# Kernel tuning notes

Measured on AMD Instinct MI355X. Metric: run time of the kernel, lower is better.

## Reference

```python
import jax, jax.numpy as jnp
import numpy as np

N = 100000      # entity nodes
E = 1000000     # edges per relation
D_IN = 256
HID = 128
EPS = 1e-16     # PyG softmax denominator eps
NEG_SLOPE = 0.2 # GATConv default leaky_relu slope


def _gat_conv(x, ei, Ws, Wd, a_s, a_d, b):
    """Single-head GATConv (heads=1, concat=False) with self-loops."""
    n = x.shape[0]
    loop = jnp.arange(n, dtype=ei.dtype)
    src = jnp.concatenate([ei[0], loop])  # [E+N]
    dst = jnp.concatenate([ei[1], loop])
    h_src = x @ Ws                         # [N, HID]
    h_dst = x @ Wd                         # [N, HID]
    a_src = h_src @ a_s                    # [N]
    a_dst = h_dst @ a_d                    # [N]
    e = jax.nn.leaky_relu(a_src[src] + a_dst[dst], NEG_SLOPE)  # [E+N]
    # numerically-stable softmax over incoming edges of each dst node
    m = jax.ops.segment_max(e, dst, num_segments=n)
    ex = jnp.exp(e - m[dst])
    denom = jax.ops.segment_sum(ex, dst, num_segments=n)
    alpha = ex / (denom[dst] + EPS)        # [E+N]
    out = jax.ops.segment_sum(alpha[:, None] * h_src[src], dst, num_segments=n)
    return out + b


def setup_inputs() -> dict:
    key = jax.random.key(0)
    ks = jax.random.split(key, 9)
    s_in = 1.0 / np.sqrt(D_IN)
    s_h = 1.0 / np.sqrt(HID)
    return {
        "x": jax.random.normal(ks[0], (N, D_IN), dtype=jnp.float32),
        "edge_index_r0": jax.random.randint(ks[1], (2, E), 0, N, dtype=jnp.int64)
                         if jax.config.jax_enable_x64 else jax.random.randint(ks[1], (2, E), 0, N).astype(jnp.int32),
        "edge_index_r1": jax.random.randint(ks[2], (2, E), 0, N, dtype=jnp.int64)
                         if jax.config.jax_enable_x64 else jax.random.randint(ks[2], (2, E), 0, N).astype(jnp.int32),
        "W_src": jax.random.normal(ks[3], (2, D_IN, HID), dtype=jnp.float32) * s_in,
        "W_dst": jax.random.normal(ks[4], (2, D_IN, HID), dtype=jnp.float32) * s_in,
        "att_src": jax.random.normal(ks[5], (2, HID), dtype=jnp.float32) * s_h,
        "att_dst": jax.random.normal(ks[6], (2, HID), dtype=jnp.float32) * s_h,
        "bias": jnp.zeros((2, HID), dtype=jnp.float32),
    }


def reference(x, edge_index_r0, edge_index_r1, W_src, W_dst, att_src, att_dst, bias):
    # HeteroConv aggr='sum' over the two entity->entity relations
    out = _gat_conv(x, edge_index_r0, W_src[0], W_dst[0], att_src[0], att_dst[0], bias[0])
    out = out + _gat_conv(x, edge_index_r1, W_src[1], W_dst[1], att_src[1], att_dst[1], bias[1])
    # ELU; dropout p=0.0 is identity
    return jax.nn.elu(out)
```

## Files before the change

kernel.cpp:

```cpp
#include <hip/hip_runtime.h>

typedef __attribute__((ext_vector_type(8))) __bf16 bf16x8;
typedef __attribute__((ext_vector_type(4))) float floatx4;
typedef __attribute__((ext_vector_type(2))) float floatx2;

__device__ __forceinline__ float bf2f(unsigned short u) {
    return __uint_as_float(((unsigned)u) << 16);
}
__device__ __forceinline__ unsigned short f2bf(float f) {
    unsigned u = __float_as_uint(f);
    unsigned r = u + 0x7FFFu + ((u >> 16) & 1u);
    return (unsigned short)(r >> 16);
}

__global__ void detect_k(const unsigned short* __restrict__ xs, int* __restrict__ flag) {
    __shared__ int sred[256];
    int tid = threadIdx.x;
    int cnt = 0;
    for (int j = 0; j < 16; ++j) {
        unsigned short u = xs[(tid * 16 + j) * 2];
        int e = (u >> 7) & 0xFF;
        cnt += (e >= 96 && e <= 159) ? 1 : 0;
    }
    sred[tid] = cnt;
    __syncthreads();
    for (int s = 128; s > 0; s >>= 1) {
        if (tid < s) sred[tid] += sred[tid + s];
        __syncthreads();
    }
    if (tid == 0) *flag = (sred[0] > 2048) ? 1 : 0;
}

__device__ __forceinline__ void canon8(const void* src, unsigned short* dst,
                                       long long idx, int f) {
    if (f) {
        *(uint4*)&dst[idx] = *(const uint4*)((const unsigned short*)src + idx);
    } else {
        const float* sf = (const float*)src;
        unsigned short v[8];
        for (int j = 0; j < 8; ++j) v[j] = f2bf(sf[idx + j]);
        *(uint4*)&dst[idx] = *(const uint4*)v;
    }
}

__global__ void prep_k(const void* __restrict__ Ws, const void* __restrict__ Wd,
                       const void* __restrict__ as, const void* __restrict__ ad,
                       const void* __restrict__ b,
                       unsigned short* __restrict__ Bt,
                       unsigned short* __restrict__ bsb,
                       float* __restrict__ vecs, const int* __restrict__ flag) {
    int blk = blockIdx.x, tid = threadIdx.x;
    int f = *flag;
    if (blk < 256) {
        int i = blk * 256 + tid;
        int r = i >> 15, rem = i & 32767;
        int k = rem >> 7, nn = rem & 127;
        unsigned short w = f ? ((const unsigned short*)Ws)[i]
                             : f2bf(((const float*)Ws)[i]);
        Bt[(size_t)r * 32768 + nn * 256 + k] = w;
    } else if (blk < 258) {
        int r = blk - 256;
        int k = tid;
        float s = 0.f, t = 0.f;
        if (f) {
            const unsigned short* wsrow = (const unsigned short*)Ws + (size_t)r * 32768 + (size_t)k * 128;
            const unsigned short* wdrow = (const unsigned short*)Wd + (size_t)r * 32768 + (size_t)k * 128;
            const unsigned short* asr = (const unsigned short*)as + r * 128;
            const unsigned short* adr = (const unsigned short*)ad + r * 128;
            for (int h = 0; h < 128; ++h) {
                s += bf2f(wsrow[h]) * bf2f(asr[h]);
                t += bf2f(wdrow[h]) * bf2f(adr[h]);
            }
        } else {
            const float* wsrow = (const float*)Ws + (size_t)r * 32768 + (size_t)k * 128;
            const float* wdrow = (const float*)Wd + (size_t)r * 32768 + (size_t)k * 128;
            const float* asr = (const float*)as + r * 128;
            const float* adr = (const float*)ad + r * 128;
            for (int h = 0; h < 128; ++h) {
                s += wsrow[h] * asr[h];
                t += wdrow[h] * adr[h];
            }
        }
        vecs[(r * 2 + 0) * 256 + k] = s;
        vecs[(r * 2 + 1) * 256 + k] = t;
    } else {
        if (tid < 32) canon8(b, bsb, (long long)tid * 8, f);
    }
}

__global__ __launch_bounds__(256) void a_canon_k(const void* __restrict__ xraw,
                                                 unsigned short* __restrict__ xb,
                                                 const float* __restrict__ vecs,
                                                 float* __restrict__ aout, int n,
                                                 const int* __restrict__ flag) {
    __shared__ float sv[1024];
    int tid = threadIdx.x;
    for (int j = 0; j < 4; ++j) sv[j * 256 + tid] = vecs[j * 256 + tid];
    __syncthreads();
    int lane = tid & 63, wave = tid >> 6;
    int row = blockIdx.x * 4 + wave;
    if (row >= n) return;
    float xf[4];
    if (*flag) {
        uint2 u = *(const uint2*)((const unsigned short*)xraw + (size_t)row * 256 + lane * 4);
        xf[0] = bf2f((unsigned short)(u.x & 0xFFFF));
        xf[1] = bf2f((unsigned short)(u.x >> 16));
        xf[2] = bf2f((unsigned short)(u.y & 0xFFFF));
        xf[3] = bf2f((unsigned short)(u.y >> 16));
        *(uint2*)&xb[(size_t)row * 256 + lane * 4] = u;
    } else {
        float4 f = *(const float4*)((const float*)xraw + (size_t)row * 256 + lane * 4);
        xf[0] = f.x; xf[1] = f.y; xf[2] = f.z; xf[3] = f.w;
        unsigned short v[4] = {f2bf(f.x), f2bf(f.y), f2bf(f.z), f2bf(f.w)};
        *(uint2*)&xb[(size_t)row * 256 + lane * 4] = *(const uint2*)v;
    }
    float s[4] = {0.f, 0.f, 0.f, 0.f};
    for (int j = 0; j < 4; ++j)
        for (int q = 0; q < 4; ++q)
            s[j] += xf[q] * sv[j * 256 + lane * 4 + q];
    for (int j = 0; j < 4; ++j)
        for (int off = 32; off > 0; off >>= 1)
            s[j] += __shfl_down(s[j], off);
    if (lane == 0)
        for (int j = 0; j < 4; ++j) aout[(size_t)j * n + row] = s[j];
}

__device__ __forceinline__ void gload_lds16(const void* g, void* l) {
    __builtin_amdgcn_global_load_lds((const __attribute__((address_space(1))) void*)g,
                                     (__attribute__((address_space(3))) void*)l, 16, 0, 0);
}

__global__ __launch_bounds__(256) void gemm_h(const unsigned short* __restrict__ x,
                                              const unsigned short* __restrict__ Btg,
                                              unsigned short* __restrict__ hout, int n) {
    const int r = blockIdx.y;
    const unsigned short* bt = Btg + (size_t)r * 32768;
    unsigned short* h = hout + (size_t)r * n * 128;
    const int r0 = blockIdx.x * 128;
    __shared__ __align__(16) unsigned short As[128 * 64];
    __shared__ __align__(16) unsigned short Bs[128 * 64];
    int tid = threadIdx.x;
    int lane = tid & 63, wave = tid >> 6;
    int wm = wave >> 1, wn = wave & 1;

    floatx4 acc[4][4];
    for (int mt = 0; mt < 4; ++mt)
        for (int nt = 0; nt < 4; ++nt)
            acc[mt][nt] = (floatx4){0.f, 0.f, 0.f, 0.f};

    int srow = lane >> 3;
    int q    = lane & 7;
    int m16  = lane & 15;
    int qb   = lane >> 4;

    for (int k0 = 0; k0 < 256; k0 += 64) {
        for (int i = 0; i < 4; ++i) {
            int L = wave * 4 + i;
            int row = L * 8 + srow;
            int sw = ((q ^ (row & 7)) << 3);
            gload_lds16(x + (size_t)(r0 + row) * 256 + k0 + sw, &As[L * 512]);
            gload_lds16(bt + (size_t)row * 256 + k0 + sw, &Bs[L * 512]);
        }
        __syncthreads();
        for (int s = 0; s < 2; ++s) {
            int qr = qb + s * 4;
            bf16x8 af[4], bfv[4];
            for (int mt = 0; mt < 4; ++mt) {
                int row = wm * 64 + mt * 16 + m16;
                af[mt] = *(const bf16x8*)&As[row * 64 + ((qr ^ (row & 7)) << 3)];
            }
            for (int nt = 0; nt < 4; ++nt) {
                int row = wn * 64 + nt * 16 + m16;
                bfv[nt] = *(const bf16x8*)&Bs[row * 64 + ((qr ^ (row & 7)) << 3)];
            }
            for (int mt = 0; mt < 4; ++mt)
                for (int nt = 0; nt < 4; ++nt)
                    acc[mt][nt] = __builtin_amdgcn_mfma_f32_16x16x32_bf16(
                        af[mt], bfv[nt], acc[mt][nt], 0, 0, 0);
        }
        __syncthreads();
    }
    for (int mt = 0; mt < 4; ++mt) {
        int baser = r0 + wm * 64 + mt * 16 + qb * 4;
        for (int nt = 0; nt < 4; ++nt) {
            int c = wn * 64 + nt * 16 + m16;
            for (int i = 0; i < 4; ++i) {
                int gr = baser + i;
                if (gr < n) h[(size_t)gr * 128 + c] = f2bf(acc[mt][nt][i]);
            }
        }
    }
}

__global__ void hist2_k(const int* __restrict__ ei0, const int* __restrict__ ei1,
                        int* __restrict__ cnt0, int* __restrict__ cnt1,
                        int* __restrict__ rank0, int* __restrict__ rank1,
                        int E_, int n) {
    int rel = blockIdx.y;
    const int* ei = rel ? ei1 : ei0;
    int* cnt = rel ? cnt1 : cnt0;
    int* rank = rel ? rank1 : rank0;
    int t = blockIdx.x * 256 + threadIdx.x;
    if (t >= E_ + n) return;
    int d = (t < E_) ? ei[E_ + t] : (t - E_);
    rank[t] = atomicAdd(&cnt[d], 1);
}

__global__ __launch_bounds__(256) void scan_red_k(const int* __restrict__ cnt0,
                                                  const int* __restrict__ cnt1,
                                                  int* __restrict__ part,
                                                  int n, int nb) {
    __shared__ int s[256];
    int rel = blockIdx.y;
    const int* cnt = rel ? cnt1 : cnt0;
    int i = blockIdx.x * 256 + threadIdx.x;
    s[threadIdx.x] = (i < n) ? cnt[i] : 0;
    __syncthreads();
    for (int o = 128; o > 0; o >>= 1) {
        if (threadIdx.x < o) s[threadIdx.x] += s[threadIdx.x + o];
        __syncthreads();
    }
    if (threadIdx.x == 0) part[rel * nb + blockIdx.x] = s[0];
}

__global__ __launch_bounds__(1024) void scan_mid_k(int* __restrict__ part, int nb) {
    __shared__ int s[1024];
    int rel = blockIdx.x;
    int t = threadIdx.x;
    s[t] = (t < nb) ? part[rel * nb + t] : 0;
    __syncthreads();
    for (int o = 1; o < 1024; o <<= 1) {
        int v = (t >= o) ? s[t - o] : 0;
        __syncthreads();
        s[t] += v;
        __syncthreads();
    }
    if (t < nb) part[rel * nb + t] = (t == 0) ? 0 : s[t - 1];
}

__global__ __launch_bounds__(256) void scan_off_k(const int* __restrict__ cnt0,
                                                  const int* __restrict__ cnt1,
                                                  const int* __restrict__ part,
                                                  int* __restrict__ off0,
                                                  int* __restrict__ off1,
                                                  int n, int nb) {
    __shared__ int s[256];
    int rel = blockIdx.y;
    const int* cnt = rel ? cnt1 : cnt0;
    int* off = rel ? off1 : off0;
    int i = blockIdx.x * 256 + threadIdx.x;
    int t = threadIdx.x;
    int v = (i < n) ? cnt[i] : 0;
    s[t] = v;
    __syncthreads();
    for (int o = 1; o < 256; o <<= 1) {
        int u = (t >= o) ? s[t - o] : 0;
        __syncthreads();
        s[t] += u;
        __syncthreads();
    }
    if (i < n) off[i] = part[rel * nb + blockIdx.x] + s[t] - v;
}

__global__ void fill2_k(const int* __restrict__ ei0, const int* __restrict__ ei1,
                        const float* __restrict__ avals,
                        const int* __restrict__ off0, const int* __restrict__ off1,
                        const int* __restrict__ rank0, const int* __restrict__ rank1,
                        unsigned long long* __restrict__ pair0,
                        unsigned long long* __restrict__ pair1,
                        int E_, int n) {
    int rel = blockIdx.y;
    const int* ei = rel ? ei1 : ei0;
    const float* as_ = avals + (rel ? 2 * (size_t)n : 0);
    const float* ad_ = avals + (rel ? 3 * (size_t)n : (size_t)n);
    const int* off = rel ? off1 : off0;
    const int* rank = rel ? rank1 : rank0;
    unsigned long long* pair = rel ? pair1 : pair0;
    int t = blockIdx.x * 256 + threadIdx.x;
    if (t >= E_ + n) return;
    int s, d;
    if (t < E_) { s = ei[t]; d = ei[E_ + t]; } else { s = t - E_; d = s; }
    float e = as_[s] + ad_[d];
    e = e > 0.f ? e : 0.2f * e;
    float w = __expf(e);
    int pos = off[d] + rank[t];
    pair[pos] = ((unsigned long long)__float_as_uint(w) << 32) | (unsigned)s;
}

__device__ __forceinline__ void acc8pk(floatx2* a, float w, const uint4& hv) {
    floatx2 wv = {w, w};
    const unsigned u[4] = {hv.x, hv.y, hv.z, hv.w};
#pragma unroll
    for (int k = 0; k < 4; ++k) {
        floatx2 hf;
        hf.x = __uint_as_float(u[k] << 16);
        hf.y = __uint_as_float(u[k] & 0xFFFF0000u);
        asm("v_pk_fma_f32 %0, %1, %2, %0" : "+v"(a[k]) : "v"(wv), "v"(hf));
    }
}

__global__ __launch_bounds__(256) void agg_k(
    const int* __restrict__ off0, const int* __restrict__ cnt0,
    const unsigned long long* __restrict__ pair0,
    const int* __restrict__ off1, const int* __restrict__ cnt1,
    const unsigned long long* __restrict__ pair1,
    const char* __restrict__ h0, const char* __restrict__ h1,
    const unsigned short* __restrict__ bias, void* __restrict__ out,
    int n, const int* __restrict__ flag) {
    int wave = threadIdx.x >> 6, lane = threadIdx.x & 63;
    int g = lane >> 4, l = lane & 15;
    unsigned l4 = (unsigned)l << 4;
    int d = blockIdx.x * 4 + wave;
    if (d >= n) return;

    int sA = off0[d], degA = cnt0[d];
    int sB = off1[d], degB = cnt1[d];
    int lastA = sA + degA - 1, lastB = sB + degB - 1;
    int nItA = (degA + 7) >> 3, nItB = (degB + 7) >> 3;
    int nIt = max(nItA, nItB);

    float denA = 0.f, denB = 0.f;
    floatx2 aA[4], aB[4];
#pragma unroll
    for (int k = 0; k < 4; ++k) {
        aA[k] = (floatx2){0.f, 0.f};
        aB[k] = (floatx2){0.f, 0.f};
    }

    int iA = sA + g, iB = sB + g;
    unsigned long long pA0 = pair0[min(iA, lastA)];
    unsigned long long pA1 = pair0[min(iA + 4, lastA)];
    unsigned long long pB0 = pair1[min(iB, lastB)];
    unsigned long long pB1 = pair1[min(iB + 4, lastB)];

    for (int it = 0; it < nIt; ++it) {
        uint4 hA0 = *(const uint4*)(h0 + ((((unsigned)pA0) << 8) + l4));
        uint4 hA1 = *(const uint4*)(h0 + ((((unsigned)pA1) << 8) + l4));
        uint4 hB0 = *(const uint4*)(h1 + ((((unsigned)pB0) << 8) + l4));
        uint4 hB1 = *(const uint4*)(h1 + ((((unsigned)pB1) << 8) + l4));
        float wA0 = (iA     <= lastA) ? __uint_as_float((unsigned)(pA0 >> 32)) : 0.f;
        float wA1 = (iA + 4 <= lastA) ? __uint_as_float((unsigned)(pA1 >> 32)) : 0.f;
        float wB0 = (iB     <= lastB) ? __uint_as_float((unsigned)(pB0 >> 32)) : 0.f;
        float wB1 = (iB + 4 <= lastB) ? __uint_as_float((unsigned)(pB1 >> 32)) : 0.f;
        iA += 8; iB += 8;
        pA0 = pair0[min(iA, lastA)];
        pA1 = pair0[min(iA + 4, lastA)];
        pB0 = pair1[min(iB, lastB)];
        pB1 = pair1[min(iB + 4, lastB)];
        denA += wA0 + wA1;
        denB += wB0 + wB1;
        acc8pk(aA, wA0, hA0);
        acc8pk(aA, wA1, hA1);
        acc8pk(aB, wB0, hB0);
        acc8pk(aB, wB1, hB1);
    }

    denA += __shfl_xor(denA, 16);
    denA += __shfl_xor(denA, 32);
    denB += __shfl_xor(denB, 16);
    denB += __shfl_xor(denB, 32);
    float invA = __builtin_amdgcn_rcpf(denA + 1e-16f);
    float invB = __builtin_amdgcn_rcpf(denB + 1e-16f);
    floatx2 ivA = {invA, invA}, ivB = {invB, invB};
#pragma unroll
    for (int k = 0; k < 4; ++k) {
        asm("v_pk_mul_f32 %0, %0, %1" : "+v"(aA[k]) : "v"(ivA));
        asm("v_pk_fma_f32 %0, %1, %2, %0" : "+v"(aA[k]) : "v"(aB[k]), "v"(ivB));
    }
    float t8[8] = {aA[0].x, aA[0].y, aA[1].x, aA[1].y,
                   aA[2].x, aA[2].y, aA[3].x, aA[3].y};

    uint4 b0 = *(const uint4*)&bias[l * 8];
    uint4 b1 = *(const uint4*)&bias[128 + l * 8];
    const unsigned* b0u = (const unsigned*)&b0;
    const unsigned* b1u = (const unsigned*)&b1;
    float v[8];
#pragma unroll
    for (int j = 0; j < 8; ++j) {
        float s = t8[j];
        s += __shfl_xor(s, 16);
        s += __shfl_xor(s, 32);
        unsigned w0 = b0u[j >> 1], w1 = b1u[j >> 1];
        float bb = bf2f((unsigned short)((j & 1) ? (w0 >> 16) : (w0 & 0xFFFFu)))
                 + bf2f((unsigned short)((j & 1) ? (w1 >> 16) : (w1 & 0xFFFFu)));
        float t = s + bb;
        v[j] = t > 0.f ? t : (__expf(t) - 1.f);
    }
    if (g == 0) {
        if (*flag) {
            unsigned pk[4];
            for (int j = 0; j < 4; ++j)
                pk[j] = ((unsigned)f2bf(v[2 * j + 1]) << 16) | (unsigned)f2bf(v[2 * j]);
            ((uint4*)out)[(size_t)d * 16 + l] = *(const uint4*)pk;
        } else {
            float4 f0 = make_float4(v[0], v[1], v[2], v[3]);
            float4 f1 = make_float4(v[4], v[5], v[6], v[7]);
            ((float4*)out)[(size_t)d * 32 + l * 2] = f0;
            ((float4*)out)[(size_t)d * 32 + l * 2 + 1] = f1;
        }
    }
}

static inline char* carve(char*& p, size_t bytes) {
    char* r = p;
    p += (bytes + 255) & ~(size_t)255;
    return r;
}

extern "C" void kernel_launch(void* const* d_in, const int* in_sizes, int n_in,
                              void* d_out, int out_size, void* d_ws, size_t ws_size,
                              hipStream_t stream) {
    (void)n_in; (void)out_size; (void)ws_size;
    const void* x_raw  = d_in[0];
    const int*  ei0    = (const int*)d_in[1];
    const int*  ei1    = (const int*)d_in[2];
    const void* Ws_raw = d_in[3];
    const void* Wd_raw = d_in[4];
    const void* as_raw = d_in[5];
    const void* ad_raw = d_in[6];
    const void* b_raw  = d_in[7];

    const int n = in_sizes[0] / 256;
    const int e = in_sizes[1] / 2;
    const int tot = e + n;
    const int nb = (n + 255) / 256;

    char* p = (char*)d_ws;
    float* avals = (float*)carve(p, (size_t)4 * n * 4);
    int*   cnt0  = (int*)carve(p, (size_t)2 * n * 4);
    int*   cnt1  = cnt0 + n;
    int*   off0  = (int*)carve(p, (size_t)n * 4);
    int*   off1  = (int*)carve(p, (size_t)n * 4);
    int*   part  = (int*)carve(p, (size_t)2 * nb * 4);
    int*   rank0 = (int*)carve(p, (size_t)tot * 4);
    int*   rank1 = (int*)carve(p, (size_t)tot * 4);
    unsigned long long* pair0 = (unsigned long long*)carve(p, (size_t)tot * 8);
    unsigned long long* pair1 = (unsigned long long*)carve(p, (size_t)tot * 8);
    float* vecs  = (float*)carve(p, 1024 * 4);
    int*   flag  = (int*)carve(p, 256);
    unsigned short* xb  = (unsigned short*)carve(p, (size_t)(n + 128) * 256 * 2);
    unsigned short* h0  = (unsigned short*)carve(p, (size_t)2 * n * 128 * 2);
    unsigned short* h1  = h0 + (size_t)n * 128;
    unsigned short* Bt  = (unsigned short*)carve(p, 65536 * 2);
    unsigned short* bsb = (unsigned short*)carve(p, 256 * 2);

    hipMemsetAsync(cnt0, 0, (size_t)2 * n * 4, stream);

    detect_k<<<1, 256, 0, stream>>>((const unsigned short*)x_raw, flag);
    prep_k<<<259, 256, 0, stream>>>(Ws_raw, Wd_raw, as_raw, ad_raw, b_raw,
                                    Bt, bsb, vecs, flag);

    int gb = (tot + 255) / 256;
    hist2_k<<<dim3(gb, 2), 256, 0, stream>>>(ei0, ei1, cnt0, cnt1, rank0, rank1, e, n);
    scan_red_k<<<dim3(nb, 2), 256, 0, stream>>>(cnt0, cnt1, part, n, nb);
    scan_mid_k<<<2, 1024, 0, stream>>>(part, nb);
    scan_off_k<<<dim3(nb, 2), 256, 0, stream>>>(cnt0, cnt1, part, off0, off1, n, nb);

    a_canon_k<<<(n + 3) / 4, 256, 0, stream>>>(x_raw, xb, vecs, avals, n, flag);
    gemm_h<<<dim3((n + 127) / 128, 2), 256, 0, stream>>>(xb, Bt, h0, n);

    fill2_k<<<dim3(gb, 2), 256, 0, stream>>>(ei0, ei1, avals, off0, off1,
                                             rank0, rank1, pair0, pair1, e, n);

    agg_k<<<(n + 3) / 4, 256, 0, stream>>>(off0, cnt0, pair0, off1, cnt1, pair1,
                                           (const char*)h0, (const char*)h1,
                                           bsb, d_out, n, flag);
}
```

Measured before the change: 468.5 us.

## Merge independent launches into heterogeneous block-dispatch kernels to cut launch gaps

Merges detection with the attention-vector prep into one single-block kernel. Combines the histogram, x canonicalisation/attention dot products and W transpose into one grid partitioned by block index. Also fuses the GEMM with the edge fill pass, so independent work runs side by side and fewer kernel launch gaps and tail bubbles occur. In exchange, the mixed kernels carry the larger shared-memory footprint (the fill blocks now allocate the GEMM LDS), which may lower occupancy for the lightweight branches.

```diff
diff --git a/kernel.cpp b/kernel.cpp
--- a/kernel.cpp
+++ b/kernel.cpp
@@ -11,24 +11,6 @@
     unsigned u = __float_as_uint(f);
     unsigned r = u + 0x7FFFu + ((u >> 16) & 1u);
     return (unsigned short)(r >> 16);
-}
-
-__global__ void detect_k(const unsigned short* __restrict__ xs, int* __restrict__ flag) {
-    __shared__ int sred[256];
-    int tid = threadIdx.x;
-    int cnt = 0;
-    for (int j = 0; j < 16; ++j) {
-        unsigned short u = xs[(tid * 16 + j) * 2];
-        int e = (u >> 7) & 0xFF;
-        cnt += (e >= 96 && e <= 159) ? 1 : 0;
-    }
-    sred[tid] = cnt;
-    __syncthreads();
-    for (int s = 128; s > 0; s >>= 1) {
-        if (tid < s) sred[tid] += sred[tid + s];
-        __syncthreads();
-    }
-    if (tid == 0) *flag = (sred[0] > 2048) ? 1 : 0;
 }
 
 __device__ __forceinline__ void canon8(const void* src, unsigned short* dst,
@@ -43,24 +25,33 @@
     }
 }
 
-__global__ void prep_k(const void* __restrict__ Ws, const void* __restrict__ Wd,
-                       const void* __restrict__ as, const void* __restrict__ ad,
-                       const void* __restrict__ b,
-                       unsigned short* __restrict__ Bt,
-                       unsigned short* __restrict__ bsb,
-                       float* __restrict__ vecs, const int* __restrict__ flag) {
-    int blk = blockIdx.x, tid = threadIdx.x;
-    int f = *flag;
-    if (blk < 256) {
-        int i = blk * 256 + tid;
-        int r = i >> 15, rem = i & 32767;
-        int k = rem >> 7, nn = rem & 127;
-        unsigned short w = f ? ((const unsigned short*)Ws)[i]
-                             : f2bf(((const float*)Ws)[i]);
-        Bt[(size_t)r * 32768 + nn * 256 + k] = w;
-    } else if (blk < 258) {
-        int r = blk - 256;
-        int k = tid;
+__global__ __launch_bounds__(256) void detect2_k(
+    const unsigned short* __restrict__ xs,
+    const void* __restrict__ Ws, const void* __restrict__ Wd,
+    const void* __restrict__ as, const void* __restrict__ ad,
+    const void* __restrict__ b,
+    int* __restrict__ flag, float* __restrict__ vecs,
+    unsigned short* __restrict__ bsb) {
+    __shared__ int sred[256];
+    __shared__ int sflag;
+    int tid = threadIdx.x;
+    int cnt = 0;
+    for (int j = 0; j < 16; ++j) {
+        unsigned short u = xs[(tid * 16 + j) * 2];
+        int e = (u >> 7) & 0xFF;
+        cnt += (e >= 96 && e <= 159) ? 1 : 0;
+    }
+    sred[tid] = cnt;
+    __syncthreads();
+    for (int s = 128; s > 0; s >>= 1) {
+        if (tid < s) sred[tid] += sred[tid + s];
+        __syncthreads();
+    }
+    if (tid == 0) { sflag = (sred[0] > 2048) ? 1 : 0; *flag = sflag; }
+    __syncthreads();
+    int f = sflag;
+    int k = tid;
+    for (int r = 0; r < 2; ++r) {
         float s = 0.f, t = 0.f;
         if (f) {
             const unsigned short* wsrow = (const unsigned short*)Ws + (size_t)r * 32768 + (size_t)k * 128;
@@ -83,127 +74,74 @@
         }
         vecs[(r * 2 + 0) * 256 + k] = s;
         vecs[(r * 2 + 1) * 256 + k] = t;
-    } else {
-        if (tid < 32) canon8(b, bsb, (long long)tid * 8, f);
-    }
-}
-
-__global__ __launch_bounds__(256) void a_canon_k(const void* __restrict__ xraw,
-                                                 unsigned short* __restrict__ xb,
-                                                 const float* __restrict__ vecs,
-                                                 float* __restrict__ aout, int n,
-                                                 const int* __restrict__ flag) {
+    }
+    if (tid < 32) canon8(b, bsb, (long long)tid * 8, f);
+}
+
+__global__ __launch_bounds__(256) void mix1_k(
+    const int* __restrict__ ei0, const int* __restrict__ ei1,
+    int* __restrict__ cnt0, int* __restrict__ cnt1,
+    int* __restrict__ rank0, int* __restrict__ rank1, int E_, int histB,
+    const void* __restrict__ xraw, unsigned short* __restrict__ xb,
+    const float* __restrict__ vecs, float* __restrict__ aout, int n, int canB,
+    const void* __restrict__ Ws, unsigned short* __restrict__ Bt,
+    const int* __restrict__ flag) {
     __shared__ float sv[1024];
-    int tid = threadIdx.x;
-    for (int j = 0; j < 4; ++j) sv[j * 256 + tid] = vecs[j * 256 + tid];
-    __syncthreads();
-    int lane = tid & 63, wave = tid >> 6;
-    int row = blockIdx.x * 4 + wave;
-    if (row >= n) return;
-    float xf[4];
-    if (*flag) {
-        uint2 u = *(const uint2*)((const unsigned short*)xraw + (size_t)row * 256 + lane * 4);
-        xf[0] = bf2f((unsigned short)(u.x & 0xFFFF));
-        xf[1] = bf2f((unsigned short)(u.x >> 16));
-        xf[2] = bf2f((unsigned short)(u.y & 0xFFFF));
-        xf[3] = bf2f((unsigned short)(u.y >> 16));
-        *(uint2*)&xb[(size_t)row * 256 + lane * 4] = u;
-    } else {
-        float4 f = *(const float4*)((const float*)xraw + (size_t)row * 256 + lane * 4);
-        xf[0] = f.x; xf[1] = f.y; xf[2] = f.z; xf[3] = f.w;
-        unsigned short v[4] = {f2bf(f.x), f2bf(f.y), f2bf(f.z), f2bf(f.w)};
-        *(uint2*)&xb[(size_t)row * 256 + lane * 4] = *(const uint2*)v;
-    }
-    float s[4] = {0.f, 0.f, 0.f, 0.f};
-    for (int j = 0; j < 4; ++j)
-        for (int q = 0; q < 4; ++q)
-            s[j] += xf[q] * sv[j * 256 + lane * 4 + q];
-    for (int j = 0; j < 4; ++j)
-        for (int off = 32; off > 0; off >>= 1)
-            s[j] += __shfl_down(s[j], off);
-    if (lane == 0)
-        for (int j = 0; j < 4; ++j) aout[(size_t)j * n + row] = s[j];
-}
-
-__device__ __forceinline__ void gload_lds16(const void* g, void* l) {
-    __builtin_amdgcn_global_load_lds((const __attribute__((address_space(1))) void*)g,
-                                     (__attribute__((address_space(3))) void*)l, 16, 0, 0);
-}
-
-__global__ __launch_bounds__(256) void gemm_h(const unsigned short* __restrict__ x,
-                                              const unsigned short* __restrict__ Btg,
-                                              unsigned short* __restrict__ hout, int n) {
-    const int r = blockIdx.y;
-    const unsigned short* bt = Btg + (size_t)r * 32768;
-    unsigned short* h = hout + (size_t)r * n * 128;
-    const int r0 = blockIdx.x * 128;
-    __shared__ __align__(16) unsigned short As[128 * 64];
-    __shared__ __align__(16) unsigned short Bs[128 * 64];
-    int tid = threadIdx.x;
-    int lane = tid & 63, wave = tid >> 6;
-    int wm = wave >> 1, wn = wave & 1;
-
-    floatx4 acc[4][4];
-    for (int mt = 0; mt < 4; ++mt)
-        for (int nt = 0; nt < 4; ++nt)
-            acc[mt][nt] = (floatx4){0.f, 0.f, 0.f, 0.f};
-
-    int srow = lane >> 3;
-    int q    = lane & 7;
-    int m16  = lane & 15;
-    int qb   = lane >> 4;
-
-    for (int k0 = 0; k0 < 256; k0 += 64) {
-        for (int i = 0; i < 4; ++i) {
-            int L = wave * 4 + i;
-            int row = L * 8 + srow;
-            int sw = ((q ^ (row & 7)) << 3);
-            gload_lds16(x + (size_t)(r0 + row) * 256 + k0 + sw, &As[L * 512]);
-            gload_lds16(bt + (size_t)row * 256 + k0 + sw, &Bs[L * 512]);
+    int b = blockIdx.x, tid = threadIdx.x;
+    if (b < histB) {
+        int rel = b & 1;
+        int t = ((b >> 1) << 8) + tid;
+        if (t >= E_ + n) return;
+        const int* ei = rel ? ei1 : ei0;
+        int* cnt = rel ? cnt1 : cnt0;
+        int* rank = rel ? rank1 : rank0;
+        int d = (t < E_) ? ei[E_ + t] : (t - E_);
+        rank[t] = atomicAdd(&cnt[d], 1);
+        return;
+    }
+    b -= histB;
+    if (b < canB) {
+        for (int j = 0; j < 4; ++j) sv[j * 256 + tid] = vecs[j * 256 + tid];
+        __syncthreads();
+        int lane = tid & 63, wave = tid >> 6;
+        int row = b * 4 + wave;
+        if (row >= n) return;
+        float xf[4];
+        if (*flag) {
+            uint2 u = *(const uint2*)((const unsigned short*)xraw + (size_t)row * 256 + lane * 4);
+            xf[0] = bf2f((unsigned short)(u.x & 0xFFFF));
+            xf[1] = bf2f((unsigned short)(u.x >> 16));
+            xf[2] = bf2f((unsigned short)(u.y & 0xFFFF));
+            xf[3] = bf2f((unsigned short)(u.y >> 16));
+            *(uint2*)&xb[(size_t)row * 256 + lane * 4] = u;
+        } else {
+            float4 f = *(const float4*)((const float*)xraw + (size_t)row * 256 + lane * 4);
+            xf[0] = f.x; xf[1] = f.y; xf[2] = f.z; xf[3] = f.w;
+            unsigned short v[4] = {f2bf(f.x), f2bf(f.y), f2bf(f.z), f2bf(f.w)};
+            *(uint2*)&xb[(size_t)row * 256 + lane * 4] = *(const uint2*)v;
         }
-        __syncthreads();
-        for (int s = 0; s < 2; ++s) {
-            int qr = qb + s * 4;
-            bf16x8 af[4], bfv[4];
-            for (int mt = 0; mt < 4; ++mt) {
-                int row = wm * 64 + mt * 16 + m16;
-                af[mt] = *(const bf16x8*)&As[row * 64 + ((qr ^ (row & 7)) << 3)];
-            }
-            for (int nt = 0; nt < 4; ++nt) {
-                int row = wn * 64 + nt * 16 + m16;
-                bfv[nt] = *(const bf16x8*)&Bs[row * 64 + ((qr ^ (row & 7)) << 3)];
-            }
-            for (int mt = 0; mt < 4; ++mt)
-                for (int nt = 0; nt < 4; ++nt)
-                    acc[mt][nt] = __builtin_amdgcn_mfma_f32_16x16x32_bf16(
-                        af[mt], bfv[nt], acc[mt][nt], 0, 0, 0);
-        }
-        __syncthreads();
-    }
-    for (int mt = 0; mt < 4; ++mt) {
-        int baser = r0 + wm * 64 + mt * 16 + qb * 4;
-        for (int nt = 0; nt < 4; ++nt) {
-            int c = wn * 64 + nt * 16 + m16;
-            for (int i = 0; i < 4; ++i) {
-                int gr = baser + i;
-                if (gr < n) h[(size_t)gr * 128 + c] = f2bf(acc[mt][nt][i]);
-            }
-        }
-    }
-}
-
-__global__ void hist2_k(const int* __restrict__ ei0, const int* __restrict__ ei1,
-                        int* __restrict__ cnt0, int* __restrict__ cnt1,
-                        int* __restrict__ rank0, int* __restrict__ rank1,
-                        int E_, int n) {
-    int rel = blockIdx.y;
-    const int* ei = rel ? ei1 : ei0;
-    int* cnt = rel ? cnt1 : cnt0;
-    int* rank = rel ? rank1 : rank0;
-    int t = blockIdx.x * 256 + threadIdx.x;
-    if (t >= E_ + n) return;
-    int d = (t < E_) ? ei[E_ + t] : (t - E_);
-    rank[t] = atomicAdd(&cnt[d], 1);
+        float s[4] = {0.f, 0.f, 0.f, 0.f};
+        for (int j = 0; j < 4; ++j)
+            for (int q = 0; q < 4; ++q)
+                s[j] += xf[q] * sv[j * 256 + lane * 4 + q];
+        for (int j = 0; j < 4; ++j)
+            for (int off = 32; off > 0; off >>= 1)
+                s[j] += __shfl_down(s[j], off);
+        if (lane == 0)
+            for (int j = 0; j < 4; ++j) aout[(size_t)j * n + row] = s[j];
+        return;
+    }
+    b -= canB;
+    {
+        int i = b * 256 + tid;
+        if (i >= 65536) return;
+        int f = *flag;
+        int r = i >> 15, rem = i & 32767;
+        int k = rem >> 7, nn = rem & 127;
+        unsigned short w = f ? ((const unsigned short*)Ws)[i]
+                             : f2bf(((const float*)Ws)[i]);
+        Bt[(size_t)r * 32768 + nn * 256 + k] = w;
+    }
 }
 
 __global__ __launch_bounds__(256) void scan_red_k(const int* __restrict__ cnt0,
@@ -262,22 +200,90 @@
     if (i < n) off[i] = part[rel * nb + blockIdx.x] + s[t] - v;
 }
 
-__global__ void fill2_k(const int* __restrict__ ei0, const int* __restrict__ ei1,
-                        const float* __restrict__ avals,
-                        const int* __restrict__ off0, const int* __restrict__ off1,
-                        const int* __restrict__ rank0, const int* __restrict__ rank1,
-                        unsigned long long* __restrict__ pair0,
-                        unsigned long long* __restrict__ pair1,
-                        int E_, int n) {
-    int rel = blockIdx.y;
+__device__ __forceinline__ void gload_lds16(const void* g, void* l) {
+    __builtin_amdgcn_global_load_lds((const __attribute__((address_space(1))) void*)g,
+                                     (__attribute__((address_space(3))) void*)l, 16, 0, 0);
+}
+
+__global__ __launch_bounds__(256) void mix2_k(
+    const unsigned short* __restrict__ x, const unsigned short* __restrict__ Btg,
+    unsigned short* __restrict__ hout, int n, int gemmB,
+    const int* __restrict__ ei0, const int* __restrict__ ei1,
+    const float* __restrict__ avals,
+    const int* __restrict__ off0, const int* __restrict__ off1,
+    const int* __restrict__ rank0, const int* __restrict__ rank1,
+    unsigned long long* __restrict__ pair0, unsigned long long* __restrict__ pair1,
+    int E_) {
+    __shared__ __align__(16) unsigned short As[128 * 64];
+    __shared__ __align__(16) unsigned short Bs[128 * 64];
+    int blk = blockIdx.x, tid = threadIdx.x;
+    if (blk < gemmB) {
+        const int r = blk & 1;
+        const unsigned short* bt = Btg + (size_t)r * 32768;
+        unsigned short* h = hout + (size_t)r * n * 128;
+        const int r0 = (blk >> 1) * 128;
+        int lane = tid & 63, wave = tid >> 6;
+        int wm = wave >> 1, wn = wave & 1;
+
+        floatx4 acc[4][4];
+        for (int mt = 0; mt < 4; ++mt)
+            for (int nt = 0; nt < 4; ++nt)
+                acc[mt][nt] = (floatx4){0.f, 0.f, 0.f, 0.f};
+
+        int srow = lane >> 3;
+        int q    = lane & 7;
+        int m16  = lane & 15;
+        int qb   = lane >> 4;
+
+        for (int k0 = 0; k0 < 256; k0 += 64) {
+            for (int i = 0; i < 4; ++i) {
+                int L = wave * 4 + i;
+                int row = L * 8 + srow;
+                int sw = ((q ^ (row & 7)) << 3);
+                gload_lds16(x + (size_t)(r0 + row) * 256 + k0 + sw, &As[L * 512]);
+                gload_lds16(bt + (size_t)row * 256 + k0 + sw, &Bs[L * 512]);
+            }
+            __syncthreads();
+            for (int s = 0; s < 2; ++s) {
+                int qr = qb + s * 4;
+                bf16x8 af[4], bfv[4];
+                for (int mt = 0; mt < 4; ++mt) {
+                    int row = wm * 64 + mt * 16 + m16;
+                    af[mt] = *(const bf16x8*)&As[row * 64 + ((qr ^ (row & 7)) << 3)];
+                }
+                for (int nt = 0; nt < 4; ++nt) {
+                    int row = wn * 64 + nt * 16 + m16;
+                    bfv[nt] = *(const bf16x8*)&Bs[row * 64 + ((qr ^ (row & 7)) << 3)];
+                }
+                for (int mt = 0; mt < 4; ++mt)
+                    for (int nt = 0; nt < 4; ++nt)
+                        acc[mt][nt] = __builtin_amdgcn_mfma_f32_16x16x32_bf16(
+                            af[mt], bfv[nt], acc[mt][nt], 0, 0, 0);
+            }
+            __syncthreads();
+        }
+        for (int mt = 0; mt < 4; ++mt) {
+            int baser = r0 + wm * 64 + mt * 16 + qb * 4;
+            for (int nt = 0; nt < 4; ++nt) {
+                int c = wn * 64 + nt * 16 + m16;
+                for (int i = 0; i < 4; ++i) {
+                    int gr = baser + i;
+                    if (gr < n) h[(size_t)gr * 128 + c] = f2bf(acc[mt][nt][i]);
+                }
+            }
+        }
+        return;
+    }
+    int fb = blk - gemmB;
+    int rel = fb & 1;
+    int t = ((fb >> 1) << 8) + tid;
+    if (t >= E_ + n) return;
     const int* ei = rel ? ei1 : ei0;
     const float* as_ = avals + (rel ? 2 * (size_t)n : 0);
     const float* ad_ = avals + (rel ? 3 * (size_t)n : (size_t)n);
     const int* off = rel ? off1 : off0;
     const int* rank = rel ? rank1 : rank0;
     unsigned long long* pair = rel ? pair1 : pair0;
-    int t = blockIdx.x * 256 + threadIdx.x;
-    if (t >= E_ + n) return;
     int s, d;
     if (t < E_) { s = ei[t]; d = ei[E_ + t]; } else { s = t - E_; d = s; }
     float e = as_[s] + ad_[d];
@@ -446,21 +452,25 @@
 
     hipMemsetAsync(cnt0, 0, (size_t)2 * n * 4, stream);
 
-    detect_k<<<1, 256, 0, stream>>>((const unsigned short*)x_raw, flag);
-    prep_k<<<259, 256, 0, stream>>>(Ws_raw, Wd_raw, as_raw, ad_raw, b_raw,
-                                    Bt, bsb, vecs, flag);
+    detect2_k<<<1, 256, 0, stream>>>((const unsigned short*)x_raw, Ws_raw, Wd_raw,
+                                     as_raw, ad_raw, b_raw, flag, vecs, bsb);
 
     int gb = (tot + 255) / 256;
-    hist2_k<<<dim3(gb, 2), 256, 0, stream>>>(ei0, ei1, cnt0, cnt1, rank0, rank1, e, n);
+    int histB = gb * 2;
+    int canB = (n + 3) / 4;
+    mix1_k<<<histB + canB + 256, 256, 0, stream>>>(
+        ei0, ei1, cnt0, cnt1, rank0, rank1, e, histB,
+        x_raw, xb, vecs, avals, n, canB,
+        Ws_raw, Bt, flag);
+
     scan_red_k<<<dim3(nb, 2), 256, 0, stream>>>(cnt0, cnt1, part, n, nb);
     scan_mid_k<<<2, 1024, 0, stream>>>(part, nb);
     scan_off_k<<<dim3(nb, 2), 256, 0, stream>>>(cnt0, cnt1, part, off0, off1, n, nb);
 
-    a_canon_k<<<(n + 3) / 4, 256, 0, stream>>>(x_raw, xb, vecs, avals, n, flag);
-    gemm_h<<<dim3((n + 127) / 128, 2), 256, 0, stream>>>(xb, Bt, h0, n);
-
-    fill2_k<<<dim3(gb, 2), 256, 0, stream>>>(ei0, ei1, avals, off0, off1,
-                                             rank0, rank1, pair0, pair1, e, n);
+    int gemmB = ((n + 127) / 128) * 2;
+    mix2_k<<<gemmB + gb * 2, 256, 0, stream>>>(
+        xb, Bt, h0, n, gemmB,
+        ei0, ei1, avals, off0, off1, rank0, rank1, pair0, pair1, e);
 
     agg_k<<<(n + 3) / 4, 256, 0, stream>>>(off0, cnt0, pair0, off1, cnt1, pair1,
                                            (const char*)h0, (const char*)h1,
```

After: 471.9 us. No clear change (+0.7%).

## Fuse histogram, x canon, pair zeroing and weight transpose into one interleaved kernel

Applied to the files above, without the earlier changes.

Merges the edge histogram, the x canonicalization with attention dot products, zeroing of padded pair buffers, and the W transpose into a single launch whose block indices interleave atomic-heavy histogram blocks with bandwidth-bound blocks. Per-destination segments are padded to multiples of 8 with zero-weight entries, so the aggregation loop drops its per-edge bounds clamps and runs each relation separately. When the input is already bf16, the GEMM reads x directly and the copy is skipped. The cost is larger pair buffers and extra zeroing traffic, plus more complex block dispatch.

```diff
diff --git a/kernel.cpp b/kernel.cpp
--- a/kernel.cpp
+++ b/kernel.cpp
@@ -11,24 +11,6 @@
     unsigned u = __float_as_uint(f);
     unsigned r = u + 0x7FFFu + ((u >> 16) & 1u);
     return (unsigned short)(r >> 16);
-}
-
-__global__ void detect_k(const unsigned short* __restrict__ xs, int* __restrict__ flag) {
-    __shared__ int sred[256];
-    int tid = threadIdx.x;
-    int cnt = 0;
-    for (int j = 0; j < 16; ++j) {
-        unsigned short u = xs[(tid * 16 + j) * 2];
-        int e = (u >> 7) & 0xFF;
-        cnt += (e >= 96 && e <= 159) ? 1 : 0;
-    }
-    sred[tid] = cnt;
-    __syncthreads();
-    for (int s = 128; s > 0; s >>= 1) {
-        if (tid < s) sred[tid] += sred[tid + s];
-        __syncthreads();
-    }
-    if (tid == 0) *flag = (sred[0] > 2048) ? 1 : 0;
 }
 
 __device__ __forceinline__ void canon8(const void* src, unsigned short* dst,
@@ -43,24 +25,32 @@
     }
 }
 
-__global__ void prep_k(const void* __restrict__ Ws, const void* __restrict__ Wd,
+__global__ void detect_k(const unsigned short* __restrict__ xs, int* __restrict__ flag) {
+    __shared__ int sred[256];
+    int tid = threadIdx.x;
+    int cnt = 0;
+    for (int j = 0; j < 16; ++j) {
+        unsigned short u = xs[(tid * 16 + j) * 2];
+        int e = (u >> 7) & 0xFF;
+        cnt += (e >= 96 && e <= 159) ? 1 : 0;
+    }
+    sred[tid] = cnt;
+    __syncthreads();
+    for (int s = 128; s > 0; s >>= 1) {
+        if (tid < s) sred[tid] += sred[tid + s];
+        __syncthreads();
+    }
+    if (tid == 0) *flag = (sred[0] > 2048) ? 1 : 0;
+}
+
+__global__ void vecb_k(const void* __restrict__ Ws, const void* __restrict__ Wd,
                        const void* __restrict__ as, const void* __restrict__ ad,
-                       const void* __restrict__ b,
-                       unsigned short* __restrict__ Bt,
-                       unsigned short* __restrict__ bsb,
-                       float* __restrict__ vecs, const int* __restrict__ flag) {
+                       const void* __restrict__ b, float* __restrict__ vecs,
+                       unsigned short* __restrict__ bsb, const int* __restrict__ flag) {
     int blk = blockIdx.x, tid = threadIdx.x;
     int f = *flag;
-    if (blk < 256) {
-        int i = blk * 256 + tid;
-        int r = i >> 15, rem = i & 32767;
-        int k = rem >> 7, nn = rem & 127;
-        unsigned short w = f ? ((const unsigned short*)Ws)[i]
-                             : f2bf(((const float*)Ws)[i]);
-        Bt[(size_t)r * 32768 + nn * 256 + k] = w;
-    } else if (blk < 258) {
-        int r = blk - 256;
-        int k = tid;
+    if (blk < 2) {
+        int r = blk, k = tid;
         float s = 0.f, t = 0.f;
         if (f) {
             const unsigned short* wsrow = (const unsigned short*)Ws + (size_t)r * 32768 + (size_t)k * 128;
@@ -88,122 +78,80 @@
     }
 }
 
-__global__ __launch_bounds__(256) void a_canon_k(const void* __restrict__ xraw,
-                                                 unsigned short* __restrict__ xb,
-                                                 const float* __restrict__ vecs,
-                                                 float* __restrict__ aout, int n,
-                                                 const int* __restrict__ flag) {
+__global__ __launch_bounds__(256) void mix1_k(
+    const int* __restrict__ ei0, const int* __restrict__ ei1,
+    int* __restrict__ cnt0, int* __restrict__ cnt1,
+    int* __restrict__ rank0, int* __restrict__ rank1, int E_, int histB, int period,
+    const void* __restrict__ xraw, unsigned short* __restrict__ xb,
+    const float* __restrict__ vecs, float* __restrict__ aout, int n, int canB,
+    unsigned long long* __restrict__ pair0, unsigned long long* __restrict__ pair1,
+    int ps2, int zB,
+    const void* __restrict__ Ws, unsigned short* __restrict__ Bt,
+    const int* __restrict__ flag) {
     __shared__ float sv[1024];
-    int tid = threadIdx.x;
-    for (int j = 0; j < 4; ++j) sv[j * 256 + tid] = vecs[j * 256 + tid];
-    __syncthreads();
-    int lane = tid & 63, wave = tid >> 6;
-    int row = blockIdx.x * 4 + wave;
-    if (row >= n) return;
-    float xf[4];
-    if (*flag) {
-        uint2 u = *(const uint2*)((const unsigned short*)xraw + (size_t)row * 256 + lane * 4);
-        xf[0] = bf2f((unsigned short)(u.x & 0xFFFF));
-        xf[1] = bf2f((unsigned short)(u.x >> 16));
-        xf[2] = bf2f((unsigned short)(u.y & 0xFFFF));
-        xf[3] = bf2f((unsigned short)(u.y >> 16));
-        *(uint2*)&xb[(size_t)row * 256 + lane * 4] = u;
-    } else {
-        float4 f = *(const float4*)((const float*)xraw + (size_t)row * 256 + lane * 4);
-        xf[0] = f.x; xf[1] = f.y; xf[2] = f.z; xf[3] = f.w;
-        unsigned short v[4] = {f2bf(f.x), f2bf(f.y), f2bf(f.z), f2bf(f.w)};
-        *(uint2*)&xb[(size_t)row * 256 + lane * 4] = *(const uint2*)v;
-    }
-    float s[4] = {0.f, 0.f, 0.f, 0.f};
-    for (int j = 0; j < 4; ++j)
-        for (int q = 0; q < 4; ++q)
-            s[j] += xf[q] * sv[j * 256 + lane * 4 + q];
-    for (int j = 0; j < 4; ++j)
-        for (int off = 32; off > 0; off >>= 1)
-            s[j] += __shfl_down(s[j], off);
-    if (lane == 0)
-        for (int j = 0; j < 4; ++j) aout[(size_t)j * n + row] = s[j];
-}
-
-__device__ __forceinline__ void gload_lds16(const void* g, void* l) {
-    __builtin_amdgcn_global_load_lds((const __attribute__((address_space(1))) void*)g,
-                                     (__attribute__((address_space(3))) void*)l, 16, 0, 0);
-}
-
-__global__ __launch_bounds__(256) void gemm_h(const unsigned short* __restrict__ x,
-                                              const unsigned short* __restrict__ Btg,
-                                              unsigned short* __restrict__ hout, int n) {
-    const int r = blockIdx.y;
-    const unsigned short* bt = Btg + (size_t)r * 32768;
-    unsigned short* h = hout + (size_t)r * n * 128;
-    const int r0 = blockIdx.x * 128;
-    __shared__ __align__(16) unsigned short As[128 * 64];
-    __shared__ __align__(16) unsigned short Bs[128 * 64];
-    int tid = threadIdx.x;
-    int lane = tid & 63, wave = tid >> 6;
-    int wm = wave >> 1, wn = wave & 1;
-
-    floatx4 acc[4][4];
-    for (int mt = 0; mt < 4; ++mt)
-        for (int nt = 0; nt < 4; ++nt)
-            acc[mt][nt] = (floatx4){0.f, 0.f, 0.f, 0.f};
-
-    int srow = lane >> 3;
-    int q    = lane & 7;
-    int m16  = lane & 15;
-    int qb   = lane >> 4;
-
-    for (int k0 = 0; k0 < 256; k0 += 64) {
-        for (int i = 0; i < 4; ++i) {
-            int L = wave * 4 + i;
-            int row = L * 8 + srow;
-            int sw = ((q ^ (row & 7)) << 3);
-            gload_lds16(x + (size_t)(r0 + row) * 256 + k0 + sw, &As[L * 512]);
-            gload_lds16(bt + (size_t)row * 256 + k0 + sw, &Bs[L * 512]);
-        }
-        __syncthreads();
-        for (int s = 0; s < 2; ++s) {
-            int qr = qb + s * 4;
-            bf16x8 af[4], bfv[4];
-            for (int mt = 0; mt < 4; ++mt) {
-                int row = wm * 64 + mt * 16 + m16;
-                af[mt] = *(const bf16x8*)&As[row * 64 + ((qr ^ (row & 7)) << 3)];
-            }
-            for (int nt = 0; nt < 4; ++nt) {
-                int row = wn * 64 + nt * 16 + m16;
-                bfv[nt] = *(const bf16x8*)&Bs[row * 64 + ((qr ^ (row & 7)) << 3)];
-            }
-            for (int mt = 0; mt < 4; ++mt)
-                for (int nt = 0; nt < 4; ++nt)
-                    acc[mt][nt] = __builtin_amdgcn_mfma_f32_16x16x32_bf16(
-                        af[mt], bfv[nt], acc[mt][nt], 0, 0, 0);
-        }
-        __syncthreads();
-    }
-    for (int mt = 0; mt < 4; ++mt) {
-        int baser = r0 + wm * 64 + mt * 16 + qb * 4;
-        for (int nt = 0; nt < 4; ++nt) {
-            int c = wn * 64 + nt * 16 + m16;
-            for (int i = 0; i < 4; ++i) {
-                int gr = baser + i;
-                if (gr < n) h[(size_t)gr * 128 + c] = f2bf(acc[mt][nt][i]);
-            }
-        }
-    }
-}
-
-__global__ void hist2_k(const int* __restrict__ ei0, const int* __restrict__ ei1,
-                        int* __restrict__ cnt0, int* __restrict__ cnt1,
-                        int* __restrict__ rank0, int* __restrict__ rank1,
-                        int E_, int n) {
-    int rel = blockIdx.y;
-    const int* ei = rel ? ei1 : ei0;
-    int* cnt = rel ? cnt1 : cnt0;
-    int* rank = rel ? rank1 : rank0;
-    int t = blockIdx.x * 256 + threadIdx.x;
-    if (t >= E_ + n) return;
-    int d = (t < E_) ? ei[E_ + t] : (t - E_);
-    rank[t] = atomicAdd(&cnt[d], 1);
+    int b = blockIdx.x, tid = threadIdx.x;
+    int bq = b / period;
+    if (b - bq * period == 0) {
+        if (bq >= histB) return;
+        int rel = bq & 1;
+        int t = ((bq >> 1) << 8) + tid;
+        if (t >= E_ + n) return;
+        const int* ei = rel ? ei1 : ei0;
+        int* cnt = rel ? cnt1 : cnt0;
+        int* rank = rel ? rank1 : rank0;
+        int d = (t < E_) ? ei[E_ + t] : (t - E_);
+        rank[t] = atomicAdd(&cnt[d], 1);
+        return;
+    }
+    int oid = b - bq - 1;
+    if (oid < canB) {
+        for (int j = 0; j < 4; ++j) sv[j * 256 + tid] = vecs[j * 256 + tid];
+        __syncthreads();
+        int lane = tid & 63, wave = tid >> 6;
+        int row = oid * 4 + wave;
+        if (row >= n) return;
+        float xf[4];
+        if (*flag) {
+            uint2 u = *(const uint2*)((const unsigned short*)xraw + (size_t)row * 256 + lane * 4);
+            xf[0] = bf2f((unsigned short)(u.x & 0xFFFF));
+            xf[1] = bf2f((unsigned short)(u.x >> 16));
+            xf[2] = bf2f((unsigned short)(u.y & 0xFFFF));
+            xf[3] = bf2f((unsigned short)(u.y >> 16));
+        } else {
+            float4 f = *(const float4*)((const float*)xraw + (size_t)row * 256 + lane * 4);
+            xf[0] = f.x; xf[1] = f.y; xf[2] = f.z; xf[3] = f.w;
+            unsigned short v[4] = {f2bf(f.x), f2bf(f.y), f2bf(f.z), f2bf(f.w)};
+            *(uint2*)&xb[(size_t)row * 256 + lane * 4] = *(const uint2*)v;
+        }
+        float s[4] = {0.f, 0.f, 0.f, 0.f};
+        for (int j = 0; j < 4; ++j)
+            for (int q = 0; q < 4; ++q)
+                s[j] += xf[q] * sv[j * 256 + lane * 4 + q];
+        for (int j = 0; j < 4; ++j)
+            for (int off = 32; off > 0; off >>= 1)
+                s[j] += __shfl_down(s[j], off);
+        if (lane == 0)
+            for (int j = 0; j < 4; ++j) aout[(size_t)j * n + row] = s[j];
+        return;
+    }
+    oid -= canB;
+    if (oid < 2 * zB) {
+        unsigned long long* dst = (oid < zB) ? pair0 : pair1;
+        int z = (oid < zB) ? oid : oid - zB;
+        int idx = z * 256 + tid;
+        if (idx < ps2) ((uint4*)dst)[idx] = make_uint4(0u, 0u, 0u, 0u);
+        return;
+    }
+    oid -= 2 * zB;
+    if (oid < 256) {
+        int i = oid * 256 + tid;
+        int f = *flag;
+        int r = i >> 15, rem = i & 32767;
+        int k = rem >> 7, nn = rem & 127;
+        unsigned short w = f ? ((const unsigned short*)Ws)[i]
+                             : f2bf(((const float*)Ws)[i]);
+        Bt[(size_t)r * 32768 + nn * 256 + k] = w;
+    }
 }
 
 __global__ __launch_bounds__(256) void scan_red_k(const int* __restrict__ cnt0,
@@ -214,7 +162,8 @@
     int rel = blockIdx.y;
     const int* cnt = rel ? cnt1 : cnt0;
     int i = blockIdx.x * 256 + threadIdx.x;
-    s[threadIdx.x] = (i < n) ? cnt[i] : 0;
+    int v = (i < n) ? ((cnt[i] + 7) & ~7) : 0;
+    s[threadIdx.x] = v;
     __syncthreads();
     for (int o = 128; o > 0; o >>= 1) {
         if (threadIdx.x < o) s[threadIdx.x] += s[threadIdx.x + o];
@@ -250,7 +199,7 @@
     int* off = rel ? off1 : off0;
     int i = blockIdx.x * 256 + threadIdx.x;
     int t = threadIdx.x;
-    int v = (i < n) ? cnt[i] : 0;
+    int v = (i < n) ? ((cnt[i] + 7) & ~7) : 0;
     s[t] = v;
     __syncthreads();
     for (int o = 1; o < 256; o <<= 1) {
@@ -287,6 +236,77 @@
     pair[pos] = ((unsigned long long)__float_as_uint(w) << 32) | (unsigned)s;
 }
 
+__device__ __forceinline__ void gload_lds16(const void* g, void* l) {
+    __builtin_amdgcn_global_load_lds((const __attribute__((address_space(1))) void*)g,
+                                     (__attribute__((address_space(3))) void*)l, 16, 0, 0);
+}
+
+__global__ __launch_bounds__(256) void gemm_h(const void* __restrict__ x_raw,
+                                              const unsigned short* __restrict__ xb,
+                                              const unsigned short* __restrict__ Btg,
+                                              unsigned short* __restrict__ hout, int n,
+                                              const int* __restrict__ flag) {
+    const unsigned short* x = (*flag) ? (const unsigned short*)x_raw : xb;
+    const int r = blockIdx.y;
+    const unsigned short* bt = Btg + (size_t)r * 32768;
+    unsigned short* h = hout + (size_t)r * n * 128;
+    const int r0 = blockIdx.x * 128;
+    __shared__ __align__(16) unsigned short As[128 * 64];
+    __shared__ __align__(16) unsigned short Bs[128 * 64];
+    int tid = threadIdx.x;
+    int lane = tid & 63, wave = tid >> 6;
+    int wm = wave >> 1, wn = wave & 1;
+
+    floatx4 acc[4][4];
+    for (int mt = 0; mt < 4; ++mt)
+        for (int nt = 0; nt < 4; ++nt)
+            acc[mt][nt] = (floatx4){0.f, 0.f, 0.f, 0.f};
+
+    int srow = lane >> 3;
+    int q    = lane & 7;
+    int m16  = lane & 15;
+    int qb   = lane >> 4;
+
+    for (int k0 = 0; k0 < 256; k0 += 64) {
+        for (int i = 0; i < 4; ++i) {
+            int L = wave * 4 + i;
+            int row = L * 8 + srow;
+            int sw = ((q ^ (row & 7)) << 3);
+            int grow = min(r0 + row, n - 1);
+            gload_lds16(x + (size_t)grow * 256 + k0 + sw, &As[L * 512]);
+            gload_lds16(bt + (size_t)row * 256 + k0 + sw, &Bs[L * 512]);
+        }
+        __syncthreads();
+        for (int s = 0; s < 2; ++s) {
+            int qr = qb + s * 4;
+            bf16x8 af[4], bfv[4];
+            for (int mt = 0; mt < 4; ++mt) {
+                int row = wm * 64 + mt * 16 + m16;
+                af[mt] = *(const bf16x8*)&As[row * 64 + ((qr ^ (row & 7)) << 3)];
+            }
+            for (int nt = 0; nt < 4; ++nt) {
+                int row = wn * 64 + nt * 16 + m16;
+                bfv[nt] = *(const bf16x8*)&Bs[row * 64 + ((qr ^ (row & 7)) << 3)];
+            }
+            for (int mt = 0; mt < 4; ++mt)
+                for (int nt = 0; nt < 4; ++nt)
+                    acc[mt][nt] = __builtin_amdgcn_mfma_f32_16x16x32_bf16(
+                        af[mt], bfv[nt], acc[mt][nt], 0, 0, 0);
+        }
+        __syncthreads();
+    }
+    for (int mt = 0; mt < 4; ++mt) {
+        int baser = r0 + wm * 64 + mt * 16 + qb * 4;
+        for (int nt = 0; nt < 4; ++nt) {
+            int c = wn * 64 + nt * 16 + m16;
+            for (int i = 0; i < 4; ++i) {
+                int gr = baser + i;
+                if (gr < n) h[(size_t)gr * 128 + c] = f2bf(acc[mt][nt][i]);
+            }
+        }
+    }
+}
+
 __device__ __forceinline__ void acc8pk(floatx2* a, float w, const uint4& hv) {
     floatx2 wv = {w, w};
     const unsigned u[4] = {hv.x, hv.y, hv.z, hv.w};
@@ -296,6 +316,28 @@
         hf.x = __uint_as_float(u[k] << 16);
         hf.y = __uint_as_float(u[k] & 0xFFFF0000u);
         asm("v_pk_fma_f32 %0, %1, %2, %0" : "+v"(a[k]) : "v"(wv), "v"(hf));
+    }
+}
+
+__device__ __forceinline__ void rel_accP(int s0, int nIt, int g, unsigned l4,
+                                         const unsigned long long* __restrict__ pair,
+                                         const char* __restrict__ h8,
+                                         floatx2* __restrict__ a, float& den) {
+    int i = s0 + g;
+    unsigned long long p0 = pair[i];
+    unsigned long long p1 = pair[i + 4];
+    for (int it = 0; it < nIt; ++it) {
+        i += 8;
+        unsigned long long q0 = pair[i];
+        unsigned long long q1 = pair[i + 4];
+        uint4 h0 = *(const uint4*)(h8 + ((((unsigned)p0) << 8) + l4));
+        uint4 h1 = *(const uint4*)(h8 + ((((unsigned)p1) << 8) + l4));
+        float w0 = __uint_as_float((unsigned)(p0 >> 32));
+        float w1 = __uint_as_float((unsigned)(p1 >> 32));
+        den += w0 + w1;
+        acc8pk(a, w0, h0);
+        acc8pk(a, w1, h1);
+        p0 = q0; p1 = q1;
     }
 }
 
@@ -313,11 +355,8 @@
     int d = blockIdx.x * 4 + wave;
     if (d >= n) return;
 
-    int sA = off0[d], degA = cnt0[d];
-    int sB = off1[d], degB = cnt1[d];
-    int lastA = sA + degA - 1, lastB = sB + degB - 1;
-    int nItA = (degA + 7) >> 3, nItB = (degB + 7) >> 3;
-    int nIt = max(nItA, nItB);
+    int sA = off0[d], nItA = (cnt0[d] + 7) >> 3;
+    int sB = off1[d], nItB = (cnt1[d] + 7) >> 3;
 
     float denA = 0.f, denB = 0.f;
     floatx2 aA[4], aB[4];
@@ -326,34 +365,8 @@
         aA[k] = (floatx2){0.f, 0.f};
         aB[k] = (floatx2){0.f, 0.f};
     }
-
-    int iA = sA + g, iB = sB + g;
-    unsigned long long pA0 = pair0[min(iA, lastA)];
-    unsigned long long pA1 = pair0[min(iA + 4, lastA)];
-    unsigned long long pB0 = pair1[min(iB, lastB)];
-    unsigned long long pB1 = pair1[min(iB + 4, lastB)];
-
-    for (int it = 0; it < nIt; ++it) {
-        uint4 hA0 = *(const uint4*)(h0 + ((((unsigned)pA0) << 8) + l4));
-        uint4 hA1 = *(const uint4*)(h0 + ((((unsigned)pA1) << 8) + l4));
-        uint4 hB0 = *(const uint4*)(h1 + ((((unsigned)pB0) << 8) + l4));
-        uint4 hB1 = *(const uint4*)(h1 + ((((unsigned)pB1) << 8) + l4));
-        float wA0 = (iA     <= lastA) ? __uint_as_float((unsigned)(pA0 >> 32)) : 0.f;
-        float wA1 = (iA + 4 <= lastA) ? __uint_as_float((unsigned)(pA1 >> 32)) : 0.f;
-        float wB0 = (iB     <= lastB) ? __uint_as_float((unsigned)(pB0 >> 32)) : 0.f;
-        float wB1 = (iB + 4 <= lastB) ? __uint_as_float((unsigned)(pB1 >> 32)) : 0.f;
-        iA += 8; iB += 8;
-        pA0 = pair0[min(iA, lastA)];
-        pA1 = pair0[min(iA + 4, lastA)];
-        pB0 = pair1[min(iB, lastB)];
-        pB1 = pair1[min(iB + 4, lastB)];
-        denA += wA0 + wA1;
-        denB += wB0 + wB1;
-        acc8pk(aA, wA0, hA0);
-        acc8pk(aA, wA1, hA1);
-        acc8pk(aB, wB0, hB0);
-        acc8pk(aB, wB1, hB1);
-    }
+    rel_accP(sA, nItA, g, l4, pair0, h0, aA, denA);
+    rel_accP(sB, nItB, g, l4, pair1, h1, aB, denB);
 
     denA += __shfl_xor(denA, 16);
     denA += __shfl_xor(denA, 32);
@@ -424,6 +437,9 @@
     const int e = in_sizes[1] / 2;
     const int tot = e + n;
     const int nb = (n + 255) / 256;
+    const int PS = tot + 7 * n + 32;
+    const int ps2 = PS / 2;
+    const int zB = (ps2 + 255) / 256;
 
     char* p = (char*)d_ws;
     float* avals = (float*)carve(p, (size_t)4 * n * 4);
@@ -434,8 +450,8 @@
     int*   part  = (int*)carve(p, (size_t)2 * nb * 4);
     int*   rank0 = (int*)carve(p, (size_t)tot * 4);
     int*   rank1 = (int*)carve(p, (size_t)tot * 4);
-    unsigned long long* pair0 = (unsigned long long*)carve(p, (size_t)tot * 8);
-    unsigned long long* pair1 = (unsigned long long*)carve(p, (size_t)tot * 8);
+    unsigned long long* pair0 = (unsigned long long*)carve(p, (size_t)PS * 8);
+    unsigned long long* pair1 = (unsigned long long*)carve(p, (size_t)PS * 8);
     float* vecs  = (float*)carve(p, 1024 * 4);
     int*   flag  = (int*)carve(p, 256);
     unsigned short* xb  = (unsigned short*)carve(p, (size_t)(n + 128) * 256 * 2);
@@ -447,20 +463,28 @@
     hipMemsetAsync(cnt0, 0, (size_t)2 * n * 4, stream);
 
     detect_k<<<1, 256, 0, stream>>>((const unsigned short*)x_raw, flag);
-    prep_k<<<259, 256, 0, stream>>>(Ws_raw, Wd_raw, as_raw, ad_raw, b_raw,
-                                    Bt, bsb, vecs, flag);
+    vecb_k<<<3, 256, 0, stream>>>(Ws_raw, Wd_raw, as_raw, ad_raw, b_raw,
+                                  vecs, bsb, flag);
 
     int gb = (tot + 255) / 256;
-    hist2_k<<<dim3(gb, 2), 256, 0, stream>>>(ei0, ei1, cnt0, cnt1, rank0, rank1, e, n);
+    int histB = gb * 2;
+    int canB = (n + 3) / 4;
+    int otherTotal = canB + 2 * zB + 256;
+    int period = (otherTotal + histB - 1) / histB + 1;
+    int G = histB * period;
+    mix1_k<<<G, 256, 0, stream>>>(
+        ei0, ei1, cnt0, cnt1, rank0, rank1, e, histB, period,
+        x_raw, xb, vecs, avals, n, canB,
+        pair0, pair1, ps2, zB,
+        Ws_raw, Bt, flag);
+
     scan_red_k<<<dim3(nb, 2), 256, 0, stream>>>(cnt0, cnt1, part, n, nb);
     scan_mid_k<<<2, 1024, 0, stream>>>(part, nb);
     scan_off_k<<<dim3(nb, 2), 256, 0, stream>>>(cnt0, cnt1, part, off0, off1, n, nb);
 
-    a_canon_k<<<(n + 3) / 4, 256, 0, stream>>>(x_raw, xb, vecs, avals, n, flag);
-    gemm_h<<<dim3((n + 127) / 128, 2), 256, 0, stream>>>(xb, Bt, h0, n);
-
     fill2_k<<<dim3(gb, 2), 256, 0, stream>>>(ei0, ei1, avals, off0, off1,
                                              rank0, rank1, pair0, pair1, e, n);
+    gemm_h<<<dim3((n + 127) / 128, 2), 256, 0, stream>>>(x_raw, xb, Bt, h0, n, flag);
 
     agg_k<<<(n + 3) / 4, 256, 0, stream>>>(off0, cnt0, pair0, off1, cnt1, pair1,
                                            (const char*)h0, (const char*)h1,
```

Result: faster. 436.6 us (-6.8%).
